# Optimization experiments

Hardware: AMD Instinct MI355X
Metric: run time of the kernel (lower is better)

The kernel has to match this reference:

```python
import jax, jax.numpy as jnp
import numpy as np

BS, SLEN, DIM, N_HEADS = 2, 2048, 2048, 16
DH = DIM // N_HEADS


def setup_inputs() -> dict:
    key = jax.random.key(0)
    ks = jax.random.split(key, 10)
    s = DIM ** -0.5
    x = jax.random.normal(ks[0], (BS, SLEN, DIM), dtype=jnp.float32)
    # causal attention mask from get_masks: True = attend
    mask = jnp.tril(jnp.ones((SLEN, SLEN), dtype=bool))[None].repeat(BS, axis=0)
    Wq = jax.random.normal(ks[1], (DIM, DIM), jnp.float32) * s
    bq = jnp.zeros((DIM,), jnp.float32)
    Wk = jax.random.normal(ks[2], (DIM, DIM), jnp.float32) * s
    bk = jnp.zeros((DIM,), jnp.float32)
    Wv = jax.random.normal(ks[3], (DIM, DIM), jnp.float32) * s
    bv = jnp.zeros((DIM,), jnp.float32)
    Wo = jax.random.normal(ks[4], (DIM, DIM), jnp.float32) * s
    bo = jnp.zeros((DIM,), jnp.float32)
    # normalized_attention learned scalar, init 1/sqrt(dim_per_head)
    scale = jnp.asarray(1.0 / np.sqrt(DH), dtype=jnp.float32)
    return {"x": x, "mask": mask, "Wq": Wq, "bq": bq, "Wk": Wk, "bk": bk,
            "Wv": Wv, "bv": bv, "Wo": Wo, "bo": bo, "scale": scale}


def _split_heads(t):  # (bs, slen, dim) -> (bs, H, slen, dh)
    return t.reshape(BS, -1, N_HEADS, DH).transpose(0, 2, 1, 3)


def reference(x, mask, Wq, bq, Wk, bk, Wv, bv, Wo, bo, scale):
    # QKV projections (torch Linear: x @ W.T + b)
    q = _split_heads(x @ Wq.T + bq)
    k = _split_heads(x @ Wk.T + bk)
    v = _split_heads(x @ Wv.T + bv)
    # normalized attention: L2-normalize q, k on head dim, learned scalar scale
    q = q / jnp.linalg.norm(q, axis=-1, keepdims=True)
    k = k / jnp.linalg.norm(k, axis=-1, keepdims=True)
    q = q * scale
    scores = jnp.einsum('bhqd,bhkd->bhqk', q, k)  # (bs, H, qlen, klen)
    scores = jnp.where(mask[:, None, :, :], scores, -jnp.inf)
    weights = jax.nn.softmax(scores, axis=-1)  # dropout p=0 / eval
    ctx = jnp.einsum('bhqk,bhkd->bhqd', weights, v)
    ctx = ctx.transpose(0, 2, 1, 3).reshape(BS, SLEN, DIM)
    return ctx @ Wo.T + bo
```

## Files before the change

kernel.cpp:

```cpp
#include <hip/hip_runtime.h>
#include <hip/hip_bf16.h>

#define S_LEN 2048
#define DIMN  2048
#define NHEAD 16
#define DHEAD 128
#define SEGQ  ((size_t)4096 * 2048)
#define SEGW  ((size_t)2048 * 2048)

typedef __attribute__((ext_vector_type(8))) short short8;
typedef __attribute__((ext_vector_type(4))) float floatx4;

__device__ inline float bf2f(unsigned short u) {
    union { unsigned int i; float f; } v; v.i = ((unsigned int)u) << 16; return v.f;
}
__device__ inline unsigned short f2bf(float f) {
    unsigned int x = __float_as_uint(f);
    unsigned int r = (x + 0x7FFFu + ((x >> 16) & 1u)) >> 16;
    return (unsigned short)r;
}
__device__ inline short8 ld8_f32_as_bf16(const float* p) {
    float4 a = *(const float4*)p;
    float4 b = *(const float4*)(p + 4);
    short8 r;
    r[0] = (short)f2bf(a.x); r[1] = (short)f2bf(a.y);
    r[2] = (short)f2bf(a.z); r[3] = (short)f2bf(a.w);
    r[4] = (short)f2bf(b.x); r[5] = (short)f2bf(b.y);
    r[6] = (short)f2bf(b.z); r[7] = (short)f2bf(b.w);
    return r;
}
__device__ inline void glds16(unsigned short* lds, const unsigned short* g) {
    __builtin_amdgcn_global_load_lds(
        (const __attribute__((address_space(1))) unsigned int*)g,
        (__attribute__((address_space(3))) unsigned int*)lds, 16, 0, 0);
}

__global__ __launch_bounds__(256) void cvt5_kernel(
    const float* __restrict__ s0, const float* __restrict__ s1,
    const float* __restrict__ s2, const float* __restrict__ s3,
    const float* __restrict__ s4,
    unsigned short* __restrict__ d0, unsigned short* __restrict__ d1,
    unsigned short* __restrict__ d2, unsigned short* __restrict__ d3,
    unsigned short* __restrict__ d4)
{
    const float* s; unsigned short* d; size_t n;
    switch (blockIdx.y) {
        case 0:  s = s0; d = d0; n = SEGQ; break;
        case 1:  s = s1; d = d1; n = SEGW; break;
        case 2:  s = s2; d = d2; n = SEGW; break;
        case 3:  s = s3; d = d3; n = SEGW; break;
        default: s = s4; d = d4; n = SEGW; break;
    }
    size_t stride = (size_t)gridDim.x * 256 * 8;
    for (size_t i = ((size_t)blockIdx.x * 256 + threadIdx.x) * 8; i < n; i += stride)
        *(short8*)&d[i] = ld8_f32_as_bf16(&s[i]);
}

#define BUFE (384 * 32)

template <int EPI>
__global__ __launch_bounds__(512) void gemm3(
    const unsigned short* __restrict__ A, const unsigned short* __restrict__ Bw,
    const float* __restrict__ b0, const float* __restrict__ b1,
    const float* __restrict__ b2, const float* __restrict__ scale_p,
    void* __restrict__ Cp, int M, int N, int K)
{
    __shared__ __align__(16) unsigned short sBuf[3 * BUFE];

    const int tid  = threadIdx.x;
    const int w    = tid >> 6, lane = tid & 63;
    const int l15  = lane & 15, quad = lane >> 4;
    const int wr   = w >> 1, wc = w & 1;
    const int tm   = blockIdx.y * 256, tn = blockIdx.x * 128;

    const int colE = ((lane & 3) * 8) ^ (((lane >> 3) & 3) << 3);
    const int cs   = (quad * 8) ^ (((l15 >> 1) & 3) << 3);
    const int srow = w * 16 + (lane >> 2);

    floatx4 acc[4][4] = {};

    auto stage = [&](int kt, int bsel) {
        const int k0 = kt * 32;
        glds16(&sBuf[bsel * BUFE + 0 * 4096 + w * 512],
               &A[(size_t)(tm + srow) * K + k0 + colE]);
        glds16(&sBuf[bsel * BUFE + 1 * 4096 + w * 512],
               &A[(size_t)(tm + 128 + srow) * K + k0 + colE]);
        glds16(&sBuf[bsel * BUFE + 8192 + w * 512],
               &Bw[(size_t)(tn + srow) * K + k0 + colE]);
    };

    const int nT = K >> 5;
    stage(0, 0);
    stage(1, 1);

    int bs = 0;
    for (int t = 0; t < nT; ++t) {
        if (t < nT - 1) asm volatile("s_waitcnt vmcnt(3)" ::: "memory");
        else            asm volatile("s_waitcnt vmcnt(0)" ::: "memory");
        __builtin_amdgcn_s_barrier();
        __builtin_amdgcn_sched_barrier(0);

        const unsigned short* bufA = &sBuf[bs * BUFE];
        const unsigned short* bufB = bufA + 8192;
        short8 af[4], bfr[4];
#pragma unroll
        for (int mi = 0; mi < 4; mi++)
            af[mi] = *(const short8*)&bufA[(wr * 64 + mi * 16 + l15) * 32 + cs];
#pragma unroll
        for (int ni = 0; ni < 4; ni++)
            bfr[ni] = *(const short8*)&bufB[(wc * 64 + ni * 16 + l15) * 32 + cs];

        if (t + 2 < nT) stage(t + 2, bs == 0 ? 2 : bs - 1);

        __builtin_amdgcn_s_setprio(1);
#pragma unroll
        for (int mi = 0; mi < 4; mi++)
#pragma unroll
            for (int ni = 0; ni < 4; ni++)
                acc[mi][ni] = __builtin_amdgcn_mfma_f32_16x16x32_bf16(af[mi], bfr[ni], acc[mi][ni], 0, 0, 0);
        __builtin_amdgcn_s_setprio(0);

        bs = (bs == 2) ? 0 : bs + 1;
    }
    __syncthreads();

    if (EPI == 0) {
        const int t = tn >> 11;
        const float* bp = (t == 0) ? b0 : (t == 1) ? b1 : b2;
        unsigned short* Q = (unsigned short*)Cp;
#pragma unroll
        for (int ni = 0; ni < 4; ni++) {
            int n = tn + wc * 64 + ni * 16 + l15;
            float bias = bp[n & 2047];
#pragma unroll
            for (int mi = 0; mi < 4; mi++)
#pragma unroll
                for (int r = 0; r < 4; r++) acc[mi][ni][r] += bias;
        }
        float ssq[4][4];
#pragma unroll
        for (int mi = 0; mi < 4; mi++)
#pragma unroll
            for (int r = 0; r < 4; r++) {
                float s = 0.0f;
#pragma unroll
                for (int ni = 0; ni < 4; ni++) s += acc[mi][ni][r] * acc[mi][ni][r];
#pragma unroll
                for (int off = 1; off < 16; off <<= 1) s += __shfl_xor(s, off, 64);
                ssq[mi][r] = s;
            }
        float* ssh = (float*)sBuf;
        if (l15 == 0) {
#pragma unroll
            for (int mi = 0; mi < 4; mi++)
#pragma unroll
                for (int r = 0; r < 4; r++)
                    ssh[wc * 256 + wr * 64 + mi * 16 + quad * 4 + r] = ssq[mi][r];
        }
        __syncthreads();
        const float scl = (t == 0) ? scale_p[0] : 1.0f;
#pragma unroll
        for (int mi = 0; mi < 4; mi++) {
            int mbase = tm + wr * 64 + mi * 16 + quad * 4;
#pragma unroll
            for (int r = 0; r < 4; r++) {
                float tot = ssq[mi][r] + ssh[(wc ^ 1) * 256 + wr * 64 + mi * 16 + quad * 4 + r];
                float f = (t < 2) ? rsqrtf(tot) * scl : 1.0f;
                int m = mbase + r;
                int b = m >> 11, s = m & 2047;
#pragma unroll
                for (int ni = 0; ni < 4; ni++) {
                    int n = tn + wc * 64 + ni * 16 + l15;
                    int h = (n >> 7) & 15, dh = n & 127;
                    float v = acc[mi][ni][r] * f;
                    size_t idx = (t < 2)
                        ? (size_t)t * SEGQ + (((size_t)(b * NHEAD + h)) * S_LEN + s) * DHEAD + dh
                        : 2 * SEGQ + (((size_t)(b * NHEAD + h)) * DHEAD + dh) * S_LEN + s;
                    Q[idx] = f2bf(v);
                }
            }
        }
    } else {
#pragma unroll
        for (int mi = 0; mi < 4; mi++) {
            int mbase = tm + wr * 64 + mi * 16 + quad * 4;
#pragma unroll
            for (int ni = 0; ni < 4; ni++) {
                int n = tn + wc * 64 + ni * 16 + l15;
                float bias = b0[n];
#pragma unroll
                for (int r = 0; r < 4; r++) {
                    int m = mbase + r;
                    ((float*)Cp)[(size_t)m * N + n] = acc[mi][ni][r] + bias;
                }
            }
        }
    }
}

template <int SPLIT, int A_F32, int OUT_F32>
__global__ __launch_bounds__(256) void gemm_bt(
    const void* __restrict__ Ap, const float* __restrict__ Bw,
    const float* __restrict__ bias, void* __restrict__ Cp,
    int M, int N, int K)
{
    __shared__ __align__(16) unsigned short sA[128 * 40];
    __shared__ __align__(16) unsigned short sB[128 * 40];

    const int tid  = threadIdx.x;
    const int w    = tid >> 6, lane = tid & 63;
    const int l15  = lane & 15, quad = lane >> 4;
    const int wm   = w >> 1, wn = w & 1;
    const int tm   = blockIdx.y * 128, tn = blockIdx.x * 128;

    const float*          Af32 = (const float*)Ap;
    const unsigned short* Abf  = (const unsigned short*)Ap;

    floatx4 acc[4][4] = {};

    for (int k0 = 0; k0 < K; k0 += 32) {
        __syncthreads();
#pragma unroll
        for (int i = 0; i < 2; i++) {
            int c   = tid + i * 256;
            int row = c >> 2;
            int kc  = (c & 3) * 8;
            size_t goff = (size_t)(tm + row) * K + k0 + kc;
            if (A_F32)
                *(short8*)&sA[row * 40 + kc] = ld8_f32_as_bf16(&Af32[goff]);
            else
                *(short8*)&sA[row * 40 + kc] = *(const short8*)&Abf[goff];
            *(short8*)&sB[row * 40 + kc] =
                ld8_f32_as_bf16(&Bw[(size_t)(tn + row) * K + k0 + kc]);
        }
        __syncthreads();

        short8 af[4], bfr[4];
#pragma unroll
        for (int mi = 0; mi < 4; mi++)
            af[mi] = *(const short8*)&sA[(wm * 64 + mi * 16 + l15) * 40 + quad * 8];
#pragma unroll
        for (int ni = 0; ni < 4; ni++)
            bfr[ni] = *(const short8*)&sB[(wn * 64 + ni * 16 + l15) * 40 + quad * 8];
#pragma unroll
        for (int mi = 0; mi < 4; mi++)
#pragma unroll
            for (int ni = 0; ni < 4; ni++)
                acc[mi][ni] = __builtin_amdgcn_mfma_f32_16x16x32_bf16(af[mi], bfr[ni], acc[mi][ni], 0, 0, 0);
    }

#pragma unroll
    for (int mi = 0; mi < 4; mi++) {
        int mbase = tm + wm * 64 + mi * 16 + quad * 4;
#pragma unroll
        for (int ni = 0; ni < 4; ni++) {
            int n = tn + wn * 64 + ni * 16 + l15;
            float bv = bias[n];
#pragma unroll
            for (int r = 0; r < 4; r++) {
                int m = mbase + r;
                float v = acc[mi][ni][r] + bv;
                if (SPLIT == 1) {
                    int b = m >> 11, s = m & 2047, h = n >> 7, dh = n & 127;
                    ((unsigned short*)Cp)[(((size_t)(b * NHEAD + h)) * S_LEN + s) * DHEAD + dh] = f2bf(v);
                } else if (SPLIT == 2) {
                    int b = m >> 11, s = m & 2047, h = n >> 7, dh = n & 127;
                    ((unsigned short*)Cp)[(((size_t)(b * NHEAD + h)) * DHEAD + dh) * S_LEN + s] = f2bf(v);
                } else if (OUT_F32) {
                    ((float*)Cp)[(size_t)m * N + n] = v;
                } else {
                    ((unsigned short*)Cp)[(size_t)m * N + n] = f2bf(v);
                }
            }
        }
    }
}

__global__ __launch_bounds__(256) void l2norm_kernel(
    unsigned short* __restrict__ qn, unsigned short* __restrict__ kn,
    const float* __restrict__ scale_p)
{
    const int w = threadIdx.x >> 6, lane = threadIdx.x & 63;
    size_t row = (size_t)blockIdx.x * 4 + w;
    unsigned short* base = (blockIdx.y == 0 ? qn : kn) + row * DHEAD;
    float a = bf2f(base[lane * 2]);
    float b = bf2f(base[lane * 2 + 1]);
    float ss = a * a + b * b;
#pragma unroll
    for (int off = 1; off < 64; off <<= 1) ss += __shfl_xor(ss, off, 64);
    float f = rsqrtf(ss);
    if (blockIdx.y == 0) f *= scale_p[0];
    base[lane * 2]     = f2bf(a * f);
    base[lane * 2 + 1] = f2bf(b * f);
}

#define KSTR  136
#define VTSTR 136
#define PSTR  136

__global__ __launch_bounds__(512) void attn_kernel4(
    const unsigned short* __restrict__ qn, const unsigned short* __restrict__ kn,
    const unsigned short* __restrict__ vt, unsigned short* __restrict__ ctx)
{
    __shared__ __align__(16) unsigned short sK [128 * KSTR];
    __shared__ __align__(16) unsigned short sVt[128 * VTSTR];
    __shared__ __align__(16) unsigned short sP [8 * 16 * PSTR];

    const int tid  = threadIdx.x;
    const int w    = tid >> 6, lane = tid & 63;
    const int l15  = lane & 15, quad = lane >> 4;
    const int xb   = blockIdx.x, bh = blockIdx.y;
    const size_t headoff = (size_t)bh * S_LEN * DHEAD;
    const unsigned short* kbase0 = kn + headoff;
    const unsigned short* vtbase = vt + headoff;
    unsigned short* sPw = sP + w * 16 * PSTR;

    short8 kpre[4], vpre[4];

    for (int half = 0; half < 2; half++) {
        const int qt = half ? (15 - xb) : xb;

        const unsigned short* qrow = qn + headoff + (size_t)(qt * 128 + w * 16 + l15) * DHEAD;
        short8 aQ[4];
#pragma unroll
        for (int ks = 0; ks < 4; ks++) aQ[ks] = *(const short8*)(qrow + ks * 32 + quad * 8);

        floatx4 O[8] = {};
        float m_i[4], l_i[4];
#pragma unroll
        for (int r = 0; r < 4; r++) { m_i[r] = -1e30f; l_i[r] = 0.0f; }

        if (half == 0) {
#pragma unroll
            for (int j = 0; j < 4; j++) {
                int c = tid + j * 512;
                kpre[j] = *(const short8*)(kbase0 + (size_t)(c >> 4) * DHEAD + (c & 15) * 8);
                vpre[j] = *(const short8*)(vtbase + (size_t)(c >> 4) * S_LEN + (c & 15) * 8);
            }
        }

        for (int kt = 0; kt <= qt; kt++) {
            __syncthreads();

#pragma unroll
            for (int j = 0; j < 4; j++) {
                int c = tid + j * 512;
                *(short8*)&sK [(c >> 4) * KSTR  + (c & 15) * 8] = kpre[j];
                *(short8*)&sVt[(c >> 4) * VTSTR + (c & 15) * 8] = vpre[j];
            }

            if (kt < qt || half == 0) {
                const int knext = (kt < qt) ? (kt + 1) * 128 : 0;
#pragma unroll
                for (int j = 0; j < 4; j++) {
                    int c = tid + j * 512;
                    kpre[j] = *(const short8*)(kbase0 + (size_t)(knext + (c >> 4)) * DHEAD + (c & 15) * 8);
                    vpre[j] = *(const short8*)(vtbase + (size_t)(c >> 4) * S_LEN + knext + (c & 15) * 8);
                }
            }
            __syncthreads();

            floatx4 sc[8] = {};
#pragma unroll
            for (int ks = 0; ks < 4; ks++) {
#pragma unroll
                for (int ni = 0; ni < 8; ni++) {
                    short8 bK = *(const short8*)&sK[(ni * 16 + l15) * KSTR + ks * 32 + quad * 8];
                    sc[ni] = __builtin_amdgcn_mfma_f32_16x16x32_bf16(aQ[ks], bK, sc[ni], 0, 0, 0);
                }
            }

            if (kt == qt) {
#pragma unroll
                for (int ni = 0; ni < 8; ni++) {
                    int cl = ni * 16 + l15;
#pragma unroll
                    for (int r = 0; r < 4; r++) {
                        int rl = w * 16 + quad * 4 + r;
                        if (cl > rl) sc[ni][r] = -1e30f;
                    }
                }
            }

            float rmax[4];
#pragma unroll
            for (int r = 0; r < 4; r++) {
                float mx = sc[0][r];
#pragma unroll
                for (int ni = 1; ni < 8; ni++) mx = fmaxf(mx, sc[ni][r]);
                rmax[r] = mx;
            }
#pragma unroll
            for (int off = 1; off < 16; off <<= 1)
#pragma unroll
                for (int r = 0; r < 4; r++) rmax[r] = fmaxf(rmax[r], __shfl_xor(rmax[r], off, 64));

            float alpha[4], rsum[4];
#pragma unroll
            for (int r = 0; r < 4; r++) {
                float mn = fmaxf(m_i[r], rmax[r]);
                alpha[r] = exp2f((m_i[r] - mn) * 1.44269504f);
                m_i[r] = mn;
                rsum[r] = 0.0f;
            }
#pragma unroll
            for (int ni = 0; ni < 8; ni++) {
#pragma unroll
                for (int r = 0; r < 4; r++) {
                    float p = exp2f((sc[ni][r] - m_i[r]) * 1.44269504f);
                    rsum[r] += p;
                    sPw[(quad * 4 + r) * PSTR + ni * 16 + l15] = f2bf(p);
                }
            }
#pragma unroll
            for (int off = 1; off < 16; off <<= 1)
#pragma unroll
                for (int r = 0; r < 4; r++) rsum[r] += __shfl_xor(rsum[r], off, 64);
#pragma unroll
            for (int r = 0; r < 4; r++) l_i[r] = l_i[r] * alpha[r] + rsum[r];
#pragma unroll
            for (int t = 0; t < 8; t++)
#pragma unroll
                for (int r = 0; r < 4; r++) O[t][r] *= alpha[r];

            __syncthreads();

#pragma unroll
            for (int ks2 = 0; ks2 < 4; ks2++) {
                short8 aP = *(const short8*)&sPw[l15 * PSTR + ks2 * 32 + quad * 8];
#pragma unroll
                for (int t = 0; t < 8; t++) {
                    short8 bV = *(const short8*)&sVt[(t * 16 + l15) * VTSTR + ks2 * 32 + quad * 8];
                    O[t] = __builtin_amdgcn_mfma_f32_16x16x32_bf16(aP, bV, O[t], 0, 0, 0);
                }
            }
        }

        const int b = bh >> 4, h = bh & 15;
#pragma unroll
        for (int r = 0; r < 4; r++) {
            float inv = 1.0f / l_i[r];
            int srow = qt * 128 + w * 16 + quad * 4 + r;
            size_t rowoff = ((size_t)(b * S_LEN + srow)) * DIMN + h * DHEAD;
#pragma unroll
            for (int t = 0; t < 8; t++)
                ctx[rowoff + t * 16 + l15] = f2bf(O[t][r] * inv);
        }
    }
}

extern "C" void kernel_launch(void* const* d_in, const int* in_sizes, int n_in,
                              void* d_out, int out_size, void* d_ws, size_t ws_size,
                              hipStream_t stream)
{
    const float* x     = (const float*)d_in[0];
    const float* Wq    = (const float*)d_in[2];
    const float* bq    = (const float*)d_in[3];
    const float* Wk    = (const float*)d_in[4];
    const float* bk    = (const float*)d_in[5];
    const float* Wv    = (const float*)d_in[6];
    const float* bv    = (const float*)d_in[7];
    const float* Wo    = (const float*)d_in[8];
    const float* bo    = (const float*)d_in[9];
    const float* scale = (const float*)d_in[10];

    const int M = 4096, N = 2048, K = 2048;
    float* out = (float*)d_out;
    const size_t need = (SEGQ + 4 * SEGW + 3 * SEGQ) * sizeof(unsigned short);

    if (ws_size >= need) {
        unsigned short* xb  = (unsigned short*)d_ws;
        unsigned short* wqb = xb  + SEGQ;
        unsigned short* wkb = wqb + SEGW;
        unsigned short* wvb = wkb + SEGW;
        unsigned short* wob = wvb + SEGW;
        unsigned short* qn  = wob + SEGW;
        unsigned short* kn  = qn  + SEGQ;
        unsigned short* vtb = kn  + SEGQ;
        unsigned short* ctx = xb;

        cvt5_kernel<<<dim3(512, 5), 256, 0, stream>>>(x, Wq, Wk, Wv, Wo,
                                                      xb, wqb, wkb, wvb, wob);
        gemm3<0><<<dim3(48, 16), 512, 0, stream>>>(xb, wqb, bq, bk, bv, scale, qn, M, 6144, K);
        attn_kernel4<<<dim3(8, 32), 512, 0, stream>>>(qn, kn, vtb, ctx);
        gemm3<1><<<dim3(16, 16), 512, 0, stream>>>(ctx, wob, bo, nullptr, nullptr, nullptr, out, M, N, K);
    } else {
        unsigned short* qn  = (unsigned short*)d_ws;
        unsigned short* kn  = qn + SEGQ;
        unsigned short* vtb = kn + SEGQ;
        unsigned short* ctx = vtb + SEGQ;

        gemm_bt<1, 1, 0><<<dim3(16, 32), 256, 0, stream>>>(x, Wq, bq, qn, M, N, K);
        gemm_bt<1, 1, 0><<<dim3(16, 32), 256, 0, stream>>>(x, Wk, bk, kn, M, N, K);
        gemm_bt<2, 1, 0><<<dim3(16, 32), 256, 0, stream>>>(x, Wv, bv, vtb, M, N, K);
        l2norm_kernel<<<dim3(16384, 2), 256, 0, stream>>>(qn, kn, scale);
        attn_kernel4<<<dim3(8, 32), 512, 0, stream>>>(qn, kn, vtb, ctx);
        gemm_bt<0, 0, 1><<<dim3(16, 32), 256, 0, stream>>>(ctx, Wo, bo, out, M, N, K);
    }
}
```

Baseline: 430.2 us.

## Replace QKV projection GEMM with 256x256-tile ping-pong pipelined kernel

Adds a new fused QKV GEMM kernel with 256x256 output tiles, 64-wide K steps and double-buffered LDS. Its main loop is hand-scheduled into quarter-tile MFMA phases, with explicit barriers and waitcnts interleaving global-to-LDS loads and LDS fragment reads. The goal is more data reuse per loaded byte and better overlap of memory and MFMA work than the previous 256x128 triple-buffered kernel. In exchange it uses a larger register footprint (8x4 accumulators) and 128KB of LDS, which lowers occupancy and adds many barriers per iteration. The L2-norm, scale and head-split epilogue is carried over to the new tile shape.

```diff
diff --git a/kernel.cpp b/kernel.cpp
--- a/kernel.cpp
+++ b/kernel.cpp
@@ -34,6 +34,9 @@
         (const __attribute__((address_space(1))) unsigned int*)g,
         (__attribute__((address_space(3))) unsigned int*)lds, 16, 0, 0);
 }
+
+#define BARX()  do { __builtin_amdgcn_s_barrier(); __builtin_amdgcn_sched_barrier(0); } while (0)
+#define LGKM0() do { asm volatile("s_waitcnt lgkmcnt(0)" ::: "memory"); __builtin_amdgcn_sched_barrier(0); } while (0)
 
 __global__ __launch_bounds__(256) void cvt5_kernel(
     const float* __restrict__ s0, const float* __restrict__ s1,
@@ -56,6 +59,193 @@
         *(short8*)&d[i] = ld8_f32_as_bf16(&s[i]);
 }
 
+__global__ __launch_bounds__(512) void gemm8(
+    const unsigned short* __restrict__ A, const unsigned short* __restrict__ Bw,
+    const float* __restrict__ b0, const float* __restrict__ b1,
+    const float* __restrict__ b2, const float* __restrict__ scale_p,
+    unsigned short* __restrict__ Cp, int M, int N, int K)
+{
+    __shared__ __align__(16) unsigned short sA[2][256 * 64];
+    __shared__ __align__(16) unsigned short sB[2][256 * 64];
+
+    const int tid  = threadIdx.x;
+    const int w    = tid >> 6, lane = tid & 63;
+    const int l15  = lane & 15, quad = (lane >> 4) & 3;
+    const int wr   = w >> 2, wc = w & 3;
+    const int tm   = blockIdx.y * 256, tn = blockIdx.x * 256;
+
+    const int colE = ((lane & 7) * 8) ^ (((4 * (w & 1)) | (lane >> 4)) << 3);
+    const int swzr = ((l15 >> 1) & 7) << 3;
+    const int cs0  = (quad * 8) ^ swzr;
+    const int cs1  = (32 + quad * 8) ^ swzr;
+
+    const unsigned short* Ag = A  + (size_t)tm * K;
+    const unsigned short* Bg = Bw + (size_t)tn * K;
+
+    floatx4 acc[8][4] = {};
+    short8 aF[4][2], bF0[2][2], bF1[2][2];
+
+    auto stA = [&](int kt, int half, int buf) {
+#pragma unroll
+        for (int j = 0; j < 2; j++) {
+            int r0 = half * 128 + j * 64 + w * 8;
+            glds16(&sA[buf][r0 * 64], &Ag[(size_t)(r0 + (lane >> 3)) * K + kt * 64 + colE]);
+        }
+    };
+    auto stB = [&](int kt, int half, int buf) {
+#pragma unroll
+        for (int j = 0; j < 2; j++) {
+            int r0 = half * 128 + j * 64 + w * 8;
+            glds16(&sB[buf][r0 * 64], &Bg[(size_t)(r0 + (lane >> 3)) * K + kt * 64 + colE]);
+        }
+    };
+    auto ldA = [&](int buf, int qm) {
+#pragma unroll
+        for (int m = 0; m < 4; m++) {
+            int r = (wr * 128 + qm * 64 + m * 16 + l15) * 64;
+            aF[m][0] = *(const short8*)&sA[buf][r + cs0];
+            aF[m][1] = *(const short8*)&sA[buf][r + cs1];
+        }
+    };
+    auto ldB0 = [&](int buf) {
+#pragma unroll
+        for (int n = 0; n < 2; n++) {
+            int r = (wc * 64 + n * 16 + l15) * 64;
+            bF0[n][0] = *(const short8*)&sB[buf][r + cs0];
+            bF0[n][1] = *(const short8*)&sB[buf][r + cs1];
+        }
+    };
+    auto ldB1 = [&](int buf) {
+#pragma unroll
+        for (int n = 0; n < 2; n++) {
+            int r = (wc * 64 + 32 + n * 16 + l15) * 64;
+            bF1[n][0] = *(const short8*)&sB[buf][r + cs0];
+            bF1[n][1] = *(const short8*)&sB[buf][r + cs1];
+        }
+    };
+    auto mf = [&](int qm, const short8 (&bf)[2][2], int qn) {
+        __builtin_amdgcn_s_setprio(1);
+#pragma unroll
+        for (int m = 0; m < 4; m++)
+#pragma unroll
+            for (int n = 0; n < 2; n++) {
+                acc[qm * 4 + m][qn * 2 + n] = __builtin_amdgcn_mfma_f32_16x16x32_bf16(
+                    aF[m][0], bf[n][0], acc[qm * 4 + m][qn * 2 + n], 0, 0, 0);
+                acc[qm * 4 + m][qn * 2 + n] = __builtin_amdgcn_mfma_f32_16x16x32_bf16(
+                    aF[m][1], bf[n][1], acc[qm * 4 + m][qn * 2 + n], 0, 0, 0);
+            }
+        __builtin_amdgcn_s_setprio(0);
+    };
+
+    stB(0, 0, 0); stB(0, 1, 0); stA(0, 0, 0); stA(0, 1, 0);
+    stB(1, 0, 1); stB(1, 1, 1); stA(1, 0, 1);
+    asm volatile("s_waitcnt vmcnt(6)" ::: "memory");
+    BARX();
+
+    const int nIter = K >> 7;
+    for (int it = 0; it < nIter; ++it) {
+        const int t2 = 2 * it + 2, t3 = 2 * it + 3;
+        const bool s2 = (t2 < (K >> 6));
+        const bool s3 = (t3 < (K >> 6));
+        ldA(0, 0); ldB0(0);
+        stA(2 * it + 1, 1, 1);
+        BARX(); LGKM0();
+        mf(0, bF0, 0);
+        BARX();
+        ldB1(0);
+        BARX(); LGKM0();
+        mf(0, bF1, 1);
+        BARX();
+        ldA(0, 1);
+        if (s2) stB(t2, 0, 0);
+        BARX(); LGKM0();
+        mf(1, bF1, 1);
+        BARX();
+        if (s2) stB(t2, 1, 0);
+        BARX(); LGKM0();
+        mf(1, bF0, 0);
+        if (s2) { asm volatile("s_waitcnt vmcnt(4)" ::: "memory"); }
+        else    { asm volatile("s_waitcnt vmcnt(0)" ::: "memory"); }
+        BARX();
+        ldA(1, 0); ldB0(1);
+        if (s2) stA(t2, 0, 0);
+        BARX(); LGKM0();
+        mf(0, bF0, 0);
+        BARX();
+        ldB1(1);
+        if (s2) stA(t2, 1, 0);
+        BARX(); LGKM0();
+        mf(0, bF1, 1);
+        BARX();
+        ldA(1, 1);
+        if (s3) stB(t3, 0, 1);
+        BARX(); LGKM0();
+        mf(1, bF1, 1);
+        BARX();
+        if (s3) { stB(t3, 1, 1); stA(t3, 0, 1); }
+        BARX(); LGKM0();
+        mf(1, bF0, 0);
+        if (s3) { asm volatile("s_waitcnt vmcnt(6)" ::: "memory"); }
+        BARX();
+    }
+    __syncthreads();
+
+    const int t = tn >> 11;
+    const float* bp = (t == 0) ? b0 : (t == 1) ? b1 : b2;
+#pragma unroll
+    for (int ni = 0; ni < 4; ni++) {
+        int n = tn + wc * 64 + ni * 16 + l15;
+        float bias = bp[n & 2047];
+#pragma unroll
+        for (int mi = 0; mi < 8; mi++)
+#pragma unroll
+            for (int r = 0; r < 4; r++) acc[mi][ni][r] += bias;
+    }
+    float ssq[8][4];
+#pragma unroll
+    for (int mi = 0; mi < 8; mi++)
+#pragma unroll
+        for (int r = 0; r < 4; r++) {
+            float s = 0.0f;
+#pragma unroll
+            for (int ni = 0; ni < 4; ni++) s += acc[mi][ni][r] * acc[mi][ni][r];
+#pragma unroll
+            for (int off = 1; off < 16; off <<= 1) s += __shfl_xor(s, off, 64);
+            ssq[mi][r] = s;
+        }
+    float* ssh = (float*)&sA[0][0];
+    if (l15 == 0) {
+#pragma unroll
+        for (int mi = 0; mi < 8; mi++)
+#pragma unroll
+            for (int r = 0; r < 4; r++)
+                ssh[w * 128 + mi * 16 + quad * 4 + r] = ssq[mi][r];
+    }
+    __syncthreads();
+    const float scl = (t == 0) ? scale_p[0] : 1.0f;
+#pragma unroll
+    for (int mi = 0; mi < 8; mi++) {
+        int mbase = tm + wr * 128 + mi * 16 + quad * 4;
+#pragma unroll
+        for (int r = 0; r < 4; r++) {
+            float tot = ssq[mi][r] + ssh[(w ^ 1) * 128 + mi * 16 + quad * 4 + r];
+            float f = (t < 2) ? rsqrtf(tot) * scl : 1.0f;
+            int m = mbase + r;
+            int b = m >> 11, s = m & 2047;
+#pragma unroll
+            for (int ni = 0; ni < 4; ni++) {
+                int n = tn + wc * 64 + ni * 16 + l15;
+                int h = (n >> 7) & 15, dh = n & 127;
+                float v = acc[mi][ni][r] * f;
+                size_t idx = (t < 2)
+                    ? (size_t)t * SEGQ + (((size_t)(b * NHEAD + h)) * S_LEN + s) * DHEAD + dh
+                    : 2 * SEGQ + (((size_t)(b * NHEAD + h)) * DHEAD + dh) * S_LEN + s;
+                Cp[idx] = f2bf(v);
+            }
+        }
+    }
+}
+
 #define BUFE (384 * 32)
 
 template <int EPI>
@@ -125,61 +315,6 @@
     __syncthreads();
 
     if (EPI == 0) {
-        const int t = tn >> 11;
-        const float* bp = (t == 0) ? b0 : (t == 1) ? b1 : b2;
-        unsigned short* Q = (unsigned short*)Cp;
-#pragma unroll
-        for (int ni = 0; ni < 4; ni++) {
-            int n = tn + wc * 64 + ni * 16 + l15;
-            float bias = bp[n & 2047];
-#pragma unroll
-            for (int mi = 0; mi < 4; mi++)
-#pragma unroll
-                for (int r = 0; r < 4; r++) acc[mi][ni][r] += bias;
-        }
-        float ssq[4][4];
-#pragma unroll
-        for (int mi = 0; mi < 4; mi++)
-#pragma unroll
-            for (int r = 0; r < 4; r++) {
-                float s = 0.0f;
-#pragma unroll
-                for (int ni = 0; ni < 4; ni++) s += acc[mi][ni][r] * acc[mi][ni][r];
-#pragma unroll
-                for (int off = 1; off < 16; off <<= 1) s += __shfl_xor(s, off, 64);
-                ssq[mi][r] = s;
-            }
-        float* ssh = (float*)sBuf;
-        if (l15 == 0) {
-#pragma unroll
-            for (int mi = 0; mi < 4; mi++)
-#pragma unroll
-                for (int r = 0; r < 4; r++)
-                    ssh[wc * 256 + wr * 64 + mi * 16 + quad * 4 + r] = ssq[mi][r];
-        }
-        __syncthreads();
-        const float scl = (t == 0) ? scale_p[0] : 1.0f;
-#pragma unroll
-        for (int mi = 0; mi < 4; mi++) {
-            int mbase = tm + wr * 64 + mi * 16 + quad * 4;
-#pragma unroll
-            for (int r = 0; r < 4; r++) {
-                float tot = ssq[mi][r] + ssh[(wc ^ 1) * 256 + wr * 64 + mi * 16 + quad * 4 + r];
-                float f = (t < 2) ? rsqrtf(tot) * scl : 1.0f;
-                int m = mbase + r;
-                int b = m >> 11, s = m & 2047;
-#pragma unroll
-                for (int ni = 0; ni < 4; ni++) {
-                    int n = tn + wc * 64 + ni * 16 + l15;
-                    int h = (n >> 7) & 15, dh = n & 127;
-                    float v = acc[mi][ni][r] * f;
-                    size_t idx = (t < 2)
-                        ? (size_t)t * SEGQ + (((size_t)(b * NHEAD + h)) * S_LEN + s) * DHEAD + dh
-                        : 2 * SEGQ + (((size_t)(b * NHEAD + h)) * DHEAD + dh) * S_LEN + s;
-                    Q[idx] = f2bf(v);
-                }
-            }
-        }
     } else {
 #pragma unroll
         for (int mi = 0; mi < 4; mi++) {
@@ -481,7 +616,7 @@
 
         cvt5_kernel<<<dim3(512, 5), 256, 0, stream>>>(x, Wq, Wk, Wv, Wo,
                                                       xb, wqb, wkb, wvb, wob);
-        gemm3<0><<<dim3(48, 16), 512, 0, stream>>>(xb, wqb, bq, bk, bv, scale, qn, M, 6144, K);
+        gemm8<<<dim3(24, 16), 512, 0, stream>>>(xb, wqb, bq, bk, bv, scale, qn, M, 6144, K);
         attn_kernel4<<<dim3(8, 32), 512, 0, stream>>>(qn, kn, vtb, ctx);
         gemm3<1><<<dim3(16, 16), 512, 0, stream>>>(ctx, wob, bo, nullptr, nullptr, nullptr, out, M, N, K);
     } else {
```

Measured after the change: 435.8 us. No clear change (+1.3%).
